# Optimization experiments

Hardware: AMD Instinct MI355X
Metric: run time of the kernel (lower is better)

## Reference

```python
import jax, jax.numpy as jnp
import numpy as np

WEIGHT = 1.0  # init kwarg `weight`


def setup_inputs() -> dict:
    key = jax.random.key(0)
    k1, k2, k3 = jax.random.split(key, 3)
    network_mesh = jax.random.normal(k1, (4, 3, 32, 16, 32), dtype=jnp.float32)
    pc = jax.random.normal(k2, (4, 3, 16384), dtype=jnp.float32)
    fem_mesh = jax.random.normal(k3, (4, 3, 32, 16, 32), dtype=jnp.float32)
    return {"network_mesh": network_mesh, "pc": pc, "fem_mesh": fem_mesh}


def reference(network_mesh, pc, fem_mesh):
    B = network_mesh.shape[0]
    # top surface: [B,3,X,Z] -> [B,3,X*Z] -> [B,N,3]
    top = network_mesh[:, :, :, -1, :].reshape(B, 3, -1).transpose(0, 2, 1)
    bottom = network_mesh[:, :, :, :-1, :]
    pcp = pc.transpose(0, 2, 1)  # [B,M,3]
    # squared pairwise distances [B,M,N] via ||a||^2 + ||b||^2 - 2 a.b
    sq = (jnp.sum(pcp * pcp, axis=-1)[:, :, None]
          + jnp.sum(top * top, axis=-1)[:, None, :]
          - 2.0 * jnp.einsum('bmd,bnd->bmn', pcp, top))
    # chamfer dist2: squared distance from each pc point to nearest top point
    dist2 = jnp.min(sq, axis=-1)  # [B,M]
    fem_loss = jnp.mean((bottom - fem_mesh[:, :, :, :-1, :]) ** 2)
    return jnp.mean(dist2) + fem_loss * WEIGHT
```

## Files before the change

kernel.cpp:

```cpp
#include <hip/hip_runtime.h>
#include <hip/hip_bf16.h>
#include <float.h>


#define NM_BATCH_STRIDE 49152
#define CH_STRIDE       16384
#define NTOP            1024
#define NWAVES          16
#define TOPS_PER_WAVE   64
#define NBLK            256
#define NTHR            1024
#define FEM_PER_BLK     180

__global__ __launch_bounds__(NTHR) void meshloss_fused(
    const float* __restrict__ nm,
    const float* __restrict__ pc,
    const float* __restrict__ fem,
    float* __restrict__ ws)
{
    __shared__ __align__(16) float xs[NTOP];
    __shared__ __align__(16) float ys[NTOP];
    __shared__ __align__(16) float zs[NTOP];
    __shared__ float pm[NWAVES * 256];
    __shared__ float wsum[NWAVES];

    const int t     = threadIdx.x;
    const int b     = blockIdx.x >> 6;
    const int chunk = blockIdx.x & 63;
    const int w     = t >> 6;
    const int l     = t & 63;

    const float* nmb = nm + b * NM_BATCH_STRIDE;
    {
        const int i = t >> 5, k = t & 31;
        const int base = i * 512 + 480 + k;
        xs[t] = nmb[0 * CH_STRIDE + base];
        ys[t] = nmb[1 * CH_STRIDE + base];
        zs[t] = nmb[2 * CH_STRIDE + base];
    }

    const float* pcb = pc + b * NM_BATCH_STRIDE;
    const int m0 = chunk * 256 + l;
    float px2[4], py2[4], pz2[4], pp[4], mn[4];
    #pragma unroll
    for (int j = 0; j < 4; ++j) {
        const int m = m0 + j * 64;
        float x = pcb[m];
        float y = pcb[CH_STRIDE + m];
        float z = pcb[2 * CH_STRIDE + m];
        pp[j]  = x * x + y * y + z * z;
        px2[j] = -2.0f * x;
        py2[j] = -2.0f * y;
        pz2[j] = -2.0f * z;
        mn[j]  = FLT_MAX;
    }
    __syncthreads();

    const float4* xs4 = reinterpret_cast<const float4*>(xs);
    const float4* ys4 = reinterpret_cast<const float4*>(ys);
    const float4* zs4 = reinterpret_cast<const float4*>(zs);
    const int base4 = w * (TOPS_PER_WAVE / 4);

    #pragma unroll 2
    for (int g = 0; g < TOPS_PER_WAVE / 8; ++g) {
        float4 X0 = xs4[base4 + 2 * g];
        float4 X1 = xs4[base4 + 2 * g + 1];
        float4 Y0 = ys4[base4 + 2 * g];
        float4 Y1 = ys4[base4 + 2 * g + 1];
        float4 Z0 = zs4[base4 + 2 * g];
        float4 Z1 = zs4[base4 + 2 * g + 1];
        float tx[8] = {X0.x, X0.y, X0.z, X0.w, X1.x, X1.y, X1.z, X1.w};
        float ty[8] = {Y0.x, Y0.y, Y0.z, Y0.w, Y1.x, Y1.y, Y1.z, Y1.w};
        float tz[8] = {Z0.x, Z0.y, Z0.z, Z0.w, Z1.x, Z1.y, Z1.z, Z1.w};
        float t2[8];
        #pragma unroll
        for (int e = 0; e < 8; ++e)
            t2[e] = __builtin_fmaf(tx[e], tx[e],
                    __builtin_fmaf(ty[e], ty[e], tz[e] * tz[e]));
        #pragma unroll
        for (int j = 0; j < 4; ++j) {
            #define DISTD(e) __builtin_fmaf(px2[j], tx[e], \
                             __builtin_fmaf(py2[j], ty[e], \
                             __builtin_fmaf(pz2[j], tz[e], t2[e])))
            float d0 = DISTD(0);
            float d1 = DISTD(1);
            float d2 = DISTD(2);
            float d3 = DISTD(3);
            float d4 = DISTD(4);
            float d5 = DISTD(5);
            float d6 = DISTD(6);
            float d7 = DISTD(7);
            #undef DISTD
            mn[j] = fminf(mn[j], fminf(d0, d1));
            mn[j] = fminf(mn[j], fminf(d2, d3));
            mn[j] = fminf(mn[j], fminf(d4, d5));
            mn[j] = fminf(mn[j], fminf(d6, d7));
        }
    }

    #pragma unroll
    for (int j = 0; j < 4; ++j)
        pm[w * 256 + l + j * 64] = mn[j] + pp[j];
    __syncthreads();

    float v = 0.0f;
    if (t < 256) {
        float d = pm[t];
        #pragma unroll
        for (int ww = 1; ww < NWAVES; ++ww)
            d = fminf(d, pm[ww * 256 + t]);
        v = d * (1.0f / 65536.0f);
    } else if (t < 256 + FEM_PER_BLK) {
        const int q   = blockIdx.x * FEM_PER_BLK + (t - 256);
        const int bci = q / 120;
        const int r   = q - bci * 120;
        const int s   = bci * 128 + r;
        float4 a = reinterpret_cast<const float4*>(nm)[s];
        float4 f = reinterpret_cast<const float4*>(fem)[s];
        float dx = a.x - f.x, dy = a.y - f.y, dz = a.z - f.z, dw = a.w - f.w;
        v = (dx * dx + dy * dy + dz * dz + dw * dw) * (1.0f / 184320.0f);
    }

    for (int o = 32; o > 0; o >>= 1) v += __shfl_down(v, o, 64);
    if (l == 0) wsum[w] = v;
    __syncthreads();
    if (t == 0) {
        float s = 0.0f;
        #pragma unroll
        for (int ww = 0; ww < NWAVES; ++ww) s += wsum[ww];
        ws[blockIdx.x] = s;
    }
}

__global__ __launch_bounds__(64) void meshloss_final(
    const float* __restrict__ ws, float* __restrict__ out)
{
    const float4 a = reinterpret_cast<const float4*>(ws)[threadIdx.x];
    float v = (a.x + a.y) + (a.z + a.w);
    for (int o = 32; o > 0; o >>= 1) v += __shfl_down(v, o, 64);
    if (threadIdx.x == 0) out[0] = v;
}

extern "C" void kernel_launch(void* const* d_in, const int* in_sizes, int n_in,
                              void* d_out, int out_size, void* d_ws, size_t ws_size,
                              hipStream_t stream) {
    const float* nm  = (const float*)d_in[0];
    const float* pc  = (const float*)d_in[1];
    const float* fem = (const float*)d_in[2];
    float* out = (float*)d_out;
    float* ws  = (float*)d_ws;

    meshloss_fused<<<NBLK, NTHR, 0, stream>>>(nm, pc, fem, ws);
    meshloss_final<<<1, 64, 0, stream>>>(ws, out);
}
```

Before: 14.56 us.

## Fold final reduction into main kernel via hierarchical atomic last-block detection

Removes the separate single-block reduction kernel. Each block writes its partial sum, then increments one of 16 padded group counters; the block completing a group bumps a master counter, and the last one sums all 256 partials and writes the output. The counters are zeroed with a memset each call, which adds a stream operation in place of the removed launch and adds atomic and fence overhead at block exit.

```diff
diff --git a/kernel.cpp b/kernel.cpp
--- a/kernel.cpp
+++ b/kernel.cpp
@@ -12,17 +12,23 @@
 #define NTHR            1024
 #define FEM_PER_BLK     180
 
+#define CNT_BASE_INT    1024
+#define CNT_STRIDE      32
+#define MASTER_OFF      512
+
 __global__ __launch_bounds__(NTHR) void meshloss_fused(
     const float* __restrict__ nm,
     const float* __restrict__ pc,
     const float* __restrict__ fem,
-    float* __restrict__ ws)
+    float* __restrict__ ws,
+    float* __restrict__ out)
 {
     __shared__ __align__(16) float xs[NTOP];
     __shared__ __align__(16) float ys[NTOP];
     __shared__ __align__(16) float zs[NTOP];
     __shared__ float pm[NWAVES * 256];
     __shared__ float wsum[NWAVES];
+    __shared__ int   isLast;
 
     const int t     = threadIdx.x;
     const int b     = blockIdx.x >> 6;
@@ -124,21 +130,37 @@
     for (int o = 32; o > 0; o >>= 1) v += __shfl_down(v, o, 64);
     if (l == 0) wsum[w] = v;
     __syncthreads();
+
+    int* cnt = reinterpret_cast<int*>(ws) + CNT_BASE_INT;
     if (t == 0) {
         float s = 0.0f;
         #pragma unroll
         for (int ww = 0; ww < NWAVES; ++ww) s += wsum[ww];
         ws[blockIdx.x] = s;
+        __threadfence();
+        isLast = 0;
+        int old = __hip_atomic_fetch_add(&cnt[(blockIdx.x & 15) * CNT_STRIDE],
+                                         1, __ATOMIC_ACQ_REL,
+                                         __HIP_MEMORY_SCOPE_AGENT);
+        if (old == 15) {
+            int old2 = __hip_atomic_fetch_add(&cnt[MASTER_OFF], 1,
+                                              __ATOMIC_ACQ_REL,
+                                              __HIP_MEMORY_SCOPE_AGENT);
+            if (old2 == 15) isLast = 1;
+        }
     }
-}
+    __syncthreads();
 
-__global__ __launch_bounds__(64) void meshloss_final(
-    const float* __restrict__ ws, float* __restrict__ out)
-{
-    const float4 a = reinterpret_cast<const float4*>(ws)[threadIdx.x];
-    float v = (a.x + a.y) + (a.z + a.w);
-    for (int o = 32; o > 0; o >>= 1) v += __shfl_down(v, o, 64);
-    if (threadIdx.x == 0) out[0] = v;
+    if (isLast && t < 64) {
+        __threadfence();
+        float acc = 0.0f;
+        #pragma unroll
+        for (int h = 0; h < 4; ++h)
+            acc += __hip_atomic_load(&ws[t + h * 64], __ATOMIC_ACQUIRE,
+                                     __HIP_MEMORY_SCOPE_AGENT);
+        for (int o = 32; o > 0; o >>= 1) acc += __shfl_down(acc, o, 64);
+        if (t == 0) out[0] = acc;
+    }
 }
 
 extern "C" void kernel_launch(void* const* d_in, const int* in_sizes, int n_in,
@@ -150,6 +172,6 @@
     float* out = (float*)d_out;
     float* ws  = (float*)d_ws;
 
-    meshloss_fused<<<NBLK, NTHR, 0, stream>>>(nm, pc, fem, ws);
-    meshloss_final<<<1, 64, 0, stream>>>(ws, out);
+    hipMemsetAsync((char*)d_ws + 4096, 0, 4096, stream);
+    meshloss_fused<<<NBLK, NTHR, 0, stream>>>(nm, pc, fem, ws, out);
 }
```

After: 27.97 us. 92.0% more time.
